# Performance work log

Measured on AMD Instinct MI355X. Metric: run time of the kernel, lower is better.

Reference implementation:

```python
import jax, jax.numpy as jnp
import numpy as np

N_NODES = 50000
N_EDGES = 800000
FEAT = 96


def _linear_params(key, din, dout):
    kw, kb = jax.random.split(key)
    scale = 1.0 / np.sqrt(din)
    W = jax.random.uniform(kw, (din, dout), jnp.float32, -scale, scale)
    b = jax.random.uniform(kb, (dout,), jnp.float32, -scale, scale)
    return W, b


def setup_inputs() -> dict:
    key = jax.random.key(0)
    ks = jax.random.split(key, 10)
    x = jax.random.normal(ks[0], (N_NODES, FEAT), jnp.float32)
    pos = jax.random.normal(ks[1], (N_NODES, 3), jnp.float32)
    edge_index = jax.random.randint(ks[2], (2, N_EDGES), 0, N_NODES, jnp.int64)
    # mlp_h: 96 -> 64 -> 3 (delta shift)
    h_w0, h_b0 = _linear_params(ks[3], FEAT, 64)
    h_w1, h_b1 = _linear_params(ks[4], 64, 3)
    # mlp_f: (96+3) -> 128 -> 96 (edge MLP)
    f_w0, f_b0 = _linear_params(ks[5], FEAT + 3, 128)
    f_w1, f_b1 = _linear_params(ks[6], 128, FEAT)
    # mlp_g: 96 -> 128 -> 96 (node update)
    g_w0, g_b0 = _linear_params(ks[7], FEAT, 128)
    g_w1, g_b1 = _linear_params(ks[8], 128, FEAT)
    return dict(x=x, pos=pos, edge_index=edge_index,
                h_w0=h_w0, h_b0=h_b0, h_w1=h_w1, h_b1=h_b1,
                f_w0=f_w0, f_b0=f_b0, f_w1=f_w1, f_b1=f_b1,
                g_w0=g_w0, g_b0=g_b0, g_w1=g_w1, g_b1=g_b1)


def _mlp2(h, w0, b0, w1, b1):
    # Linear -> ReLU -> Linear (output_activation='none')
    return jax.nn.relu(h @ w0 + b0) @ w1 + b1


def reference(x, pos, edge_index,
              h_w0, h_b0, h_w1, h_b1,
              f_w0, f_b0, f_w1, f_b1,
              g_w0, g_b0, g_w1, g_b1):
    src = edge_index[0]  # j: source / neighbor
    dst = edge_index[1]  # i: target
    # delta = mlp_h(x_i): learned shift of the center position
    delta = _mlp2(x, h_w0, h_b0, h_w1, h_b1)  # [N, 3]
    # per-edge feature: cat([pos_j - pos_i + delta_i, x_j])
    rel = pos[src] - pos[dst] + delta[dst]          # [E, 3]
    e_in = jnp.concatenate([rel, x[src]], axis=1)   # [E, 3+F]
    e = _mlp2(e_in, f_w0, f_b0, f_w1, f_b1)         # [E, F]
    # max-aggregate edges to target nodes (PointGNNConv aggr='max')
    agg = jax.ops.segment_max(e, dst, num_segments=N_NODES)
    agg = jnp.where(jnp.isneginf(agg), jnp.zeros_like(agg), agg)
    # residual node update
    return x + _mlp2(agg, g_w0, g_b0, g_w1, g_b1)
```

## Files before the change

kernel.cpp:

```cpp
#include <hip/hip_runtime.h>
#include <hip/hip_bf16.h>

typedef unsigned short u16;
typedef unsigned int u32;
typedef __bf16 bf16x8 __attribute__((ext_vector_type(8)));
typedef float f32x4 __attribute__((ext_vector_type(4)));

__device__ __forceinline__ float bf2f(u16 h) { return __uint_as_float(((u32)h) << 16); }
__device__ __forceinline__ u16 f2bf(float f) {
    u32 u = __float_as_uint(f);
    u32 r = u + 0x7FFFu + ((u >> 16) & 1u);
    return (u16)(r >> 16);
}
__device__ __forceinline__ u32 cvtpk(float lo, float hi) {
    u32 r;
    asm("v_cvt_pk_bf16_f32 %0, %1, %2" : "=v"(r) : "v"(lo), "v"(hi));
    return r;
}
__device__ __forceinline__ u16 cvt1(float v) { return (u16)cvtpk(v, v); }
__device__ __forceinline__ void unpack8(const u16* p, float* b) {
    uint4 v = *(const uint4*)p;
    b[0] = bf2f((u16)(v.x & 0xFFFF)); b[1] = bf2f((u16)(v.x >> 16));
    b[2] = bf2f((u16)(v.y & 0xFFFF)); b[3] = bf2f((u16)(v.y >> 16));
    b[4] = bf2f((u16)(v.z & 0xFFFF)); b[5] = bf2f((u16)(v.z >> 16));
    b[6] = bf2f((u16)(v.w & 0xFFFF)); b[7] = bf2f((u16)(v.w >> 16));
}
__device__ __forceinline__ float ldf(int bf, const void* p, long i) {
    return bf ? bf2f(((const u16*)p)[i]) : ((const float*)p)[i];
}

__global__ void k_detect(const u32* __restrict__ x, const u32* __restrict__ ei, u32* __restrict__ flags) {
    int tid = threadIdx.x;
    int c = 0;
    for (int i = tid; i < 256; i += 64) {
        u32 e = (x[i] >> 7) & 0xFF;
        if (e >= 96 && e <= 160) c++;
    }
#pragma unroll
    for (int d = 1; d < 64; d <<= 1) c += __shfl_xor(c, d);
    int z = (ei[2 * tid + 1] == 0u) ? 1 : 0;
#pragma unroll
    for (int d = 1; d < 64; d <<= 1) z += __shfl_xor(z, d);
    if (tid == 0) {
        flags[0] = (c >= 192) ? 1u : 0u;
        flags[1] = (z >= 48) ? 1u : 0u;
    }
}

__global__ void k_prep(const void* __restrict__ fw0, const void* __restrict__ fw1,
                       const void* __restrict__ gw0, const void* __restrict__ gw1,
                       const void* __restrict__ hw0,
                       u16* __restrict__ w0t, u16* __restrict__ w1t,
                       u16* __restrict__ w0tg, u16* __restrict__ w1tg, u16* __restrict__ hw0t,
                       const u32* __restrict__ flags,
                       u32* __restrict__ z1, int nz1, u32* __restrict__ z2, int nz2) {
    int bf = (int)flags[0];
    int tid = blockIdx.x * blockDim.x + threadIdx.x;
    int stride = gridDim.x * blockDim.x;
    for (int i = tid; i < nz1; i += stride) z1[i] = 0u;
    for (int i = tid; i < nz2; i += stride) z2[i] = 0u;
    for (int i = tid; i < 128 * 128; i += stride) {
        int c = i >> 7, kp = i & 127;
        float vf = (kp < 96) ? ldf(bf, fw0, (long)(kp + 3) * 128 + c) : 0.f;
        w0t[i] = f2bf(vf);
        float vg = (kp < 96) ? ldf(bf, gw0, (long)kp * 128 + c) : 0.f;
        w0tg[i] = f2bf(vg);
    }
    for (int i = tid; i < 96 * 128; i += stride) {
        int c = i >> 7, k = i & 127;
        w1t[i]  = f2bf(ldf(bf, fw1, (long)k * 96 + c));
        w1tg[i] = f2bf(ldf(bf, gw1, (long)k * 96 + c));
    }
    for (int i = tid; i < 64 * 128; i += stride) {
        int c = i >> 7, kp = i & 127;
        float v = (kp < 96) ? ldf(bf, hw0, (long)kp * 64 + c) : 0.f;
        hw0t[i] = f2bf(v);
    }
}

__global__ void k_cvt(const u32* __restrict__ ei, u32* __restrict__ eraw, u32* __restrict__ hist,
                      const u32* __restrict__ flags, int nE, int N) {
    u32 i64f = flags[1];
    for (long e = blockIdx.x * blockDim.x + threadIdx.x; e < nE; e += (long)gridDim.x * blockDim.x) {
        int src, dst;
        if (i64f) { src = (int)ei[2 * e]; dst = (int)ei[2 * ((long)nE + e)]; }
        else      { src = (int)ei[e];     dst = (int)ei[(long)nE + e]; }
        src = min(max(src, 0), N - 1);
        dst = min(max(dst, 0), N - 1);
        eraw[e] = (u32)src | ((u32)dst << 16);
        atomicAdd(&hist[dst], 1u);
    }
}

__global__ __launch_bounds__(256)
void k_scanA(const u32* __restrict__ hist, u32* __restrict__ blkSum, int n) {
    __shared__ u32 red[4];
    int tid = threadIdx.x;
    int base = blockIdx.x * 1024 + tid * 4;
    u32 s = 0;
#pragma unroll
    for (int j = 0; j < 4; j++) {
        int idx = base + j;
        if (idx < n) s += hist[idx];
    }
#pragma unroll
    for (int d = 1; d < 64; d <<= 1) s += __shfl_xor(s, d);
    if ((tid & 63) == 0) red[tid >> 6] = s;
    __syncthreads();
    if (tid == 0) blkSum[blockIdx.x] = red[0] + red[1] + red[2] + red[3];
}
__global__ __launch_bounds__(256)
void k_scanC(const u32* __restrict__ hist, const u32* __restrict__ blkSum,
             u32* __restrict__ cur, u32* __restrict__ dstart, int n, u32 total) {
    __shared__ u32 a[256];
    int tid = threadIdx.x;
    a[tid] = (tid < blockIdx.x) ? blkSum[tid] : 0u;
    __syncthreads();
    for (int d = 128; d > 0; d >>= 1) {
        if (tid < d) a[tid] += a[tid + d];
        __syncthreads();
    }
    u32 boff = a[0];
    __syncthreads();
    int base = blockIdx.x * 1024 + tid * 4;
    u32 e[4];
    u32 ts = 0;
#pragma unroll
    for (int j = 0; j < 4; j++) {
        int idx = base + j;
        e[j] = (idx < n) ? hist[idx] : 0u;
        ts += e[j];
    }
    a[tid] = ts;
    __syncthreads();
    for (int d = 1; d < 256; d <<= 1) {
        u32 t = (tid >= d) ? a[tid - d] : 0u;
        __syncthreads();
        a[tid] += t;
        __syncthreads();
    }
    u32 off = boff + a[tid] - ts;
#pragma unroll
    for (int j = 0; j < 4; j++) {
        int idx = base + j;
        if (idx < n) { cur[idx] = off; dstart[idx] = off; off += e[j]; }
    }
    if (blockIdx.x == 0 && tid == 0) dstart[n] = total;
}

__global__ void k_scatter(const u32* __restrict__ eraw, u32* __restrict__ cur,
                          u32* __restrict__ edges, int nE) {
    for (long e = blockIdx.x * blockDim.x + threadIdx.x; e < nE; e += (long)gridDim.x * blockDim.x) {
        u32 ed = eraw[e];
        u32 p = atomicAdd(&cur[ed >> 16], 1u);
        edges[p] = ed;
    }
}

__global__ __launch_bounds__(256)
void k_yd(const void* __restrict__ x, const void* __restrict__ pos,
          const u16* __restrict__ w0t, const u16* __restrict__ hw0t,
          const void* __restrict__ hb0, const void* __restrict__ hw1, const void* __restrict__ hb1,
          const void* __restrict__ fw0, const void* __restrict__ fb0,
          u16* __restrict__ yu, float* __restrict__ vbO,
          const u32* __restrict__ flags, int N)
{
    const int bf = (int)flags[0];
    __shared__ __align__(16) char arena[16384];
    __shared__ float posS[64][4];
    __shared__ float h1S[64][68];
    __shared__ float w0rS[384];
    __shared__ float b0fS[128];
    __shared__ float hb0S[64];
    __shared__ float hw1S[192];
    __shared__ float hb1S[3];
    int tid = threadIdx.x;
    for (int i = tid; i < 384; i += 256) w0rS[i] = ldf(bf, fw0, i);
    if (tid < 128) b0fS[tid] = ldf(bf, fb0, tid);
    if (tid < 64)  hb0S[tid] = ldf(bf, hb0, tid);
    if (tid < 192) hw1S[tid] = ldf(bf, hw1, tid);
    if (tid < 3)   hb1S[tid] = ldf(bf, hb1, tid);
    __syncthreads();

    const int lane = tid & 63;
    const int wid  = tid >> 6;
    const int mrow0 = wid * 16;
    const int r16  = lane & 15;
    const int arow = mrow0 + r16;
    const int kgrp = lane >> 4;
    const int srow = tid >> 2;
    const int q = tid & 3;
    const int ssw = (srow & 7) << 4;

    int ntile = (N + 63) / 64;
    for (int t = blockIdx.x; t < ntile; t += gridDim.x) {
        {
            int n = t * 64 + srow;
            if (tid < 64) {
                int n2 = t * 64 + tid;
                posS[tid][0] = (n2 < N) ? ldf(bf, pos, (long)n2 * 3 + 0) : 0.f;
                posS[tid][1] = (n2 < N) ? ldf(bf, pos, (long)n2 * 3 + 1) : 0.f;
                posS[tid][2] = (n2 < N) ? ldf(bf, pos, (long)n2 * 3 + 2) : 0.f;
            }
            if (n < N) {
                if (bf) {
                    const uint4* ar = (const uint4*)((const u16*)x + (size_t)n * 96);
#pragma unroll
                    for (int j = 0; j < 3; j++) {
                        int c = q * 3 + j;
                        *(uint4*)(arena + srow * 256 + ((c * 16) ^ ssw)) = ar[c];
                    }
                } else {
                    const float4* xp = (const float4*)((const float*)x + (size_t)n * 96);
#pragma unroll
                    for (int j = 0; j < 3; j++) {
                        int c = q * 3 + j;
                        float4 v0 = xp[2 * c], v1 = xp[2 * c + 1];
                        *(uint4*)(arena + srow * 256 + ((c * 16) ^ ssw)) =
                            make_uint4(cvtpk(v0.x, v0.y), cvtpk(v0.z, v0.w),
                                       cvtpk(v1.x, v1.y), cvtpk(v1.z, v1.w));
                    }
                }
            } else {
#pragma unroll
                for (int j = 0; j < 3; j++)
                    *(uint4*)(arena + srow * 256 + (((q * 3 + j) * 16) ^ ssw)) = make_uint4(0u, 0u, 0u, 0u);
            }
        }
        __syncthreads();
        int sw = (arow & 7) << 4;
        bf16x8 a0 = *(const bf16x8*)(arena + arow * 256 + ((0   + kgrp * 16) ^ sw));
        bf16x8 a1 = *(const bf16x8*)(arena + arow * 256 + ((64  + kgrp * 16) ^ sw));
        bf16x8 a2 = *(const bf16x8*)(arena + arow * 256 + ((128 + kgrp * 16) ^ sw));
        f32x4 accd[4];
#pragma unroll
        for (int nt = 0; nt < 4; nt++) {
#pragma unroll
            for (int r = 0; r < 4; r++) accd[nt][r] = 0.f;
        }
#pragma unroll
        for (int nt = 0; nt < 4; nt++) {
            const u16* wp = hw0t + (long)(nt * 16 + r16) * 128 + kgrp * 8;
            accd[nt] = __builtin_amdgcn_mfma_f32_16x16x32_bf16(a0, *(const bf16x8*)(wp),      accd[nt], 0, 0, 0);
            accd[nt] = __builtin_amdgcn_mfma_f32_16x16x32_bf16(a1, *(const bf16x8*)(wp + 32), accd[nt], 0, 0, 0);
            accd[nt] = __builtin_amdgcn_mfma_f32_16x16x32_bf16(a2, *(const bf16x8*)(wp + 64), accd[nt], 0, 0, 0);
        }
#pragma unroll
        for (int nt = 0; nt < 4; nt++) {
            int col = nt * 16 + r16;
#pragma unroll
            for (int r = 0; r < 4; r++)
                h1S[mrow0 + kgrp * 4 + r][col] = fmaxf(accd[nt][r] + hb0S[col], 0.f);
        }
        f32x4 acc[8];
#pragma unroll
        for (int nt = 0; nt < 8; nt++) {
#pragma unroll
            for (int r = 0; r < 4; r++) acc[nt][r] = 0.f;
        }
#pragma unroll
        for (int nt = 0; nt < 8; nt++) {
            const u16* wp = w0t + (long)(nt * 16 + r16) * 128 + kgrp * 8;
            acc[nt] = __builtin_amdgcn_mfma_f32_16x16x32_bf16(a0, *(const bf16x8*)(wp),      acc[nt], 0, 0, 0);
            acc[nt] = __builtin_amdgcn_mfma_f32_16x16x32_bf16(a1, *(const bf16x8*)(wp + 32), acc[nt], 0, 0, 0);
            acc[nt] = __builtin_amdgcn_mfma_f32_16x16x32_bf16(a2, *(const bf16x8*)(wp + 64), acc[nt], 0, 0, 0);
        }
        __syncthreads();
        {
            int nl = tid >> 2;
            int n = t * 64 + nl;
            float d0 = hb1S[0], d1 = hb1S[1], d2 = hb1S[2];
#pragma unroll 8
            for (int j = 0; j < 64; j++) {
                float hv = h1S[nl][j];
                d0 += hv * hw1S[j * 3 + 0];
                d1 += hv * hw1S[j * 3 + 1];
                d2 += hv * hw1S[j * 3 + 2];
            }
            float p0 = d0 - posS[nl][0], p1 = d1 - posS[nl][1], p2 = d2 - posS[nl][2];
            if (n < N) {
                float* vrow = vbO + (size_t)n * 128 + q * 32;
#pragma unroll
                for (int c4 = 0; c4 < 8; c4++) {
                    float4 o;
#pragma unroll
                    for (int k = 0; k < 4; k++) {
                        int col = q * 32 + c4 * 4 + k;
                        float v = p0 * w0rS[col] + p1 * w0rS[128 + col] + p2 * w0rS[256 + col] + b0fS[col];
                        ((float*)&o)[k] = v;
                    }
                    *(float4*)(vrow + c4 * 4) = o;
                }
            }
        }
#pragma unroll
        for (int nt = 0; nt < 8; nt++) {
            int col = nt * 16 + r16;
            float wr0 = w0rS[col], wr1 = w0rS[128 + col], wr2 = w0rS[256 + col];
#pragma unroll
            for (int r = 0; r < 4; r++) {
                int row = mrow0 + kgrp * 4 + r;
                int n2 = t * 64 + row;
                if (n2 < N) {
                    float u = posS[row][0] * wr0 + posS[row][1] * wr1 + posS[row][2] * wr2;
                    yu[(size_t)n2 * 128 + col] = cvt1(acc[nt][r] + u);
                }
            }
        }
        __syncthreads();
    }
}

__global__ __launch_bounds__(256)
void k_edge(const u16* __restrict__ yu, const float4* __restrict__ vb,
            const u32* __restrict__ edges, const u16* __restrict__ w1t,
            const void* __restrict__ fb1, const u32* __restrict__ flags,
            u16* __restrict__ agg, u16* __restrict__ pbuf, int nE)
{
    const int bf = (int)flags[0];
    __shared__ __align__(16) u16 w1S[96 * 128];
    __shared__ float b1s[96];
    __shared__ int dstS[4][16];
    __shared__ __align__(16) u16 outS[4][16 * 98];
    int tid = threadIdx.x;
    for (int i = tid; i < 96 * 64; i += 256) {
        int col = i >> 6, kp = i & 63;
        u32 v = ((const u32*)w1t)[i];
        *(u32*)((char*)w1S + col * 256 + ((kp * 4) ^ ((col & 7) << 4))) = v;
    }
    if (tid < 96) b1s[tid] = ldf(bf, fb1, tid);
    __syncthreads();

    const int lane = tid & 63;
    const int wid  = tid >> 6;
    const int r16  = lane & 15;
    const int kgrp = lane >> 4;
    const int ntile = (nE + 15) / 16;
    const size_t tailSlot = (size_t)ntile * 96;
    u16* const outSw = outS[wid];

    const int stride = (int)gridDim.x * 4;
    int t = (int)blockIdx.x * 4 + wid;

    u32 ce = 0u, ne = 0u;
    uint4 G[4];

    auto issueGather = [&](u32 src) {
        const u16* yp = yu + (size_t)src * 128 + kgrp * 8;
#pragma unroll
        for (int f = 0; f < 4; f++) G[f] = *(const uint4*)(yp + f * 32);
    };

    if (t < ntile) {
        long E = min((long)t * 16 + r16, (long)nE - 1);
        ce = edges[E];
        issueGather(ce & 0xFFFFu);
        int tn = t + stride;
        if (tn < ntile) {
            long En = min((long)tn * 16 + r16, (long)nE - 1);
            ne = edges[En];
        }
    }

    for (; t < ntile; t += stride) {
        asm volatile("" ::: "memory");
        if (kgrp == 3) dstS[wid][r16] = (int)(ce >> 16);
        int dprevV = -1, dnextV = -1;
        {
            long e0 = (long)t * 16;
            if (e0 > 0) dprevV = (int)(edges[e0 - 1] >> 16);
            if (e0 + 16 < (long)nE) dnextV = (int)(edges[e0 + 16] >> 16);
        }
        const float4* vbp = vb + (size_t)(ce >> 16) * 32 + kgrp * 2;
        bf16x8 hf[4];
#pragma unroll
        for (int f = 0; f < 4; f++) {
            float4 v0 = vbp[f * 8], v1 = vbp[f * 8 + 1];
            u32 w0 = G[f].x, w1 = G[f].y, w2 = G[f].z, w3 = G[f].w;
            u32 hw[4];
            hw[0] = cvtpk(fmaxf(bf2f((u16)(w0 & 0xFFFF)) + v0.x, 0.f),
                          fmaxf(bf2f((u16)(w0 >> 16))    + v0.y, 0.f));
            hw[1] = cvtpk(fmaxf(bf2f((u16)(w1 & 0xFFFF)) + v0.z, 0.f),
                          fmaxf(bf2f((u16)(w1 >> 16))    + v0.w, 0.f));
            hw[2] = cvtpk(fmaxf(bf2f((u16)(w2 & 0xFFFF)) + v1.x, 0.f),
                          fmaxf(bf2f((u16)(w2 >> 16))    + v1.y, 0.f));
            hw[3] = cvtpk(fmaxf(bf2f((u16)(w3 & 0xFFFF)) + v1.z, 0.f),
                          fmaxf(bf2f((u16)(w3 >> 16))    + v1.w, 0.f));
            uint4 hv = make_uint4(hw[0], hw[1], hw[2], hw[3]);
            hf[f] = *(const bf16x8*)&hv;
        }
        u32 c2e = ne;
        {
            int tn = t + stride;
            if (tn < ntile) {
                issueGather(c2e & 0xFFFFu);
                int tn2 = tn + stride;
                if (tn2 < ntile) {
                    long E2 = min((long)tn2 * 16 + r16, (long)nE - 1);
                    ne = edges[E2];
                }
            }
        }
        f32x4 acc2[6];
#pragma unroll
        for (int nt = 0; nt < 6; nt++) {
#pragma unroll
            for (int r = 0; r < 4; r++) acc2[nt][r] = 0.f;
        }
#pragma unroll
        for (int nt = 0; nt < 6; nt++) {
            int colr = nt * 16 + r16;
            const char* wb = (const char*)w1S + colr * 256;
            int csw = (colr & 7) << 4;
            acc2[nt] = __builtin_amdgcn_mfma_f32_16x16x32_bf16(hf[0], *(const bf16x8*)(wb + ((kgrp * 16)       ^ csw)), acc2[nt], 0, 0, 0);
            acc2[nt] = __builtin_amdgcn_mfma_f32_16x16x32_bf16(hf[1], *(const bf16x8*)(wb + ((kgrp * 16 + 64)  ^ csw)), acc2[nt], 0, 0, 0);
            acc2[nt] = __builtin_amdgcn_mfma_f32_16x16x32_bf16(hf[2], *(const bf16x8*)(wb + ((kgrp * 16 + 128) ^ csw)), acc2[nt], 0, 0, 0);
            acc2[nt] = __builtin_amdgcn_mfma_f32_16x16x32_bf16(hf[3], *(const bf16x8*)(wb + ((kgrp * 16 + 192) ^ csw)), acc2[nt], 0, 0, 0);
        }
#pragma unroll
        for (int nt = 0; nt < 6; nt++) {
            int col = nt * 16 + r16;
#pragma unroll
            for (int r = 0; r < 4; r++) {
                int row = kgrp * 4 + r;
                outSw[row * 98 + col] = cvt1(acc2[nt][r]);
            }
        }
        {
            int d0s = dstS[wid][0], d15s = dstS[wid][15];
            bool extL = (dprevV == d0s);
            bool extR = (dnextV == d15s);
#pragma unroll
            for (int p = 0; p < 2; p++) {
                int col = p * 64 + lane;
                if (p == 0 || lane < 32) {
                    float b1c = b1s[col];
                    int curd = d0s;
                    int r0 = 0;
                    float m = bf2f(outSw[col]);
#pragma unroll
                    for (int row = 1; row < 16; row++) {
                        float v = bf2f(outSw[row * 98 + col]);
                        int d = dstS[wid][row];
                        if (d != curd) {
                            if (r0 == 0 && extL) pbuf[(size_t)t * 96 + col] = cvt1(m);
                            else agg[(size_t)curd * 96 + col] = cvt1(m + b1c);
                            curd = d; r0 = row; m = v;
                        } else m = fmaxf(m, v);
                    }
                    bool pl = (r0 == 0) && extL;
                    if (pl || extR) {
                        size_t slot = (r0 == 0) ? 0 : tailSlot;
                        pbuf[slot + (size_t)t * 96 + col] = cvt1(m);
                    } else agg[(size_t)curd * 96 + col] = cvt1(m + b1c);
                }
            }
        }
        ce = c2e;
    }
}

__global__ __launch_bounds__(256)
void k_node(const void* __restrict__ x, const u16* __restrict__ agg,
            const u32* __restrict__ dstart, const u16* __restrict__ pbuf,
            const u16* __restrict__ w0tg, const u16* __restrict__ w1tg,
            const void* __restrict__ gb0, const void* __restrict__ gb1,
            const void* __restrict__ fb1,
            void* __restrict__ out, const u32* __restrict__ flags, int N, int nE)
{
    const int bf = (int)flags[0];
    __shared__ __align__(16) char arena[32768];
    __shared__ float b0s[128];
    __shared__ float b1s[96];
    __shared__ float b1f[96];
    int tid = threadIdx.x;
    if (tid < 128) b0s[tid] = ldf(bf, gb0, tid);
    if (tid < 96)  b1s[tid] = ldf(bf, gb1, tid);
    if (tid < 96)  b1f[tid] = ldf(bf, fb1, tid);
    __syncthreads();

    const int lane = tid & 63;
    const int wid  = tid >> 6;
    const int mrow0 = wid * 16;
    const int arow = mrow0 + (lane & 15);
    const int kgrp = lane >> 4;
    const int srow = tid >> 2;
    const int q = tid & 3;
    const int ssw = (srow & 7) << 4;
    const int ntileE = (nE + 15) / 16;

    float b0v[8];
#pragma unroll
    for (int nt = 0; nt < 8; nt++) b0v[nt] = b0s[nt * 16 + (lane & 15)];

    auto outOff = [](int row, int col) {
        int j = row & 15, w2 = row >> 4;
        int base = (j < 8) ? (w2 * 4096 + j * 512) : (16384 + w2 * 4096 + (j - 8) * 512);
        return base + ((col ^ (((row >> 2) & 3) << 4)) << 2);
    };

    int ntile = (N + 63) / 64;
    for (int t = blockIdx.x; t < ntile; t += gridDim.x) {
        asm volatile("" ::: "memory");
        {
            int n = t * 64 + srow;
            if (n < N) {
                u32 s = dstart[n], e = dstart[n + 1];
                int t0 = (int)(s >> 4);
                int t1 = (e > s) ? (int)((e - 1) >> 4) : t0;
                if (e > s && t0 != t1) {
                    const u16* pH = pbuf;
                    const u16* pT = pbuf + (size_t)ntileE * 96;
                    const u16* first = ((s & 15u) == 0u) ? pH : pT;
#pragma unroll
                    for (int j = 0; j < 3; j++) {
                        int c = q * 3 + j;
                        float mf[8];
                        unpack8(first + (size_t)t0 * 96 + c * 8, mf);
                        for (int tt = t0 + 1; tt <= t1; tt++) {
                            float tf[8];
                            unpack8(pH + (size_t)tt * 96 + c * 8, tf);
#pragma unroll
                            for (int k = 0; k < 8; k++) mf[k] = fmaxf(mf[k], tf[k]);
                        }
                        uint4 o;
                        o.x = cvtpk(mf[0] + b1f[c * 8 + 0], mf[1] + b1f[c * 8 + 1]);
                        o.y = cvtpk(mf[2] + b1f[c * 8 + 2], mf[3] + b1f[c * 8 + 3]);
                        o.z = cvtpk(mf[4] + b1f[c * 8 + 4], mf[5] + b1f[c * 8 + 5]);
                        o.w = cvtpk(mf[6] + b1f[c * 8 + 6], mf[7] + b1f[c * 8 + 7]);
                        *(uint4*)(arena + srow * 256 + ((c * 16) ^ ssw)) = o;
                    }
                } else {
                    const uint4* ar = (const uint4*)(agg + (size_t)n * 96);
#pragma unroll
                    for (int j = 0; j < 3; j++) {
                        int c = q * 3 + j;
                        *(uint4*)(arena + srow * 256 + ((c * 16) ^ ssw)) = ar[c];
                    }
                }
            } else {
#pragma unroll
                for (int j = 0; j < 3; j++)
                    *(uint4*)(arena + srow * 256 + (((q * 3 + j) * 16) ^ ssw)) = make_uint4(0u, 0u, 0u, 0u);
            }
        }
        __syncthreads();
        int sw = (arow & 7) << 4;
        bf16x8 a0 = *(const bf16x8*)(arena + arow * 256 + ((0   + kgrp * 16) ^ sw));
        bf16x8 a1 = *(const bf16x8*)(arena + arow * 256 + ((64  + kgrp * 16) ^ sw));
        bf16x8 a2 = *(const bf16x8*)(arena + arow * 256 + ((128 + kgrp * 16) ^ sw));
        f32x4 acc[8];
#pragma unroll
        for (int nt = 0; nt < 8; nt++) {
#pragma unroll
            for (int r = 0; r < 4; r++) acc[nt][r] = 0.f;
        }
#pragma unroll
        for (int nt = 0; nt < 8; nt++) {
            const u16* wp = w0tg + (long)(nt * 16 + (lane & 15)) * 128 + kgrp * 8;
            acc[nt] = __builtin_amdgcn_mfma_f32_16x16x32_bf16(a0, *(const bf16x8*)(wp),      acc[nt], 0, 0, 0);
            acc[nt] = __builtin_amdgcn_mfma_f32_16x16x32_bf16(a1, *(const bf16x8*)(wp + 32), acc[nt], 0, 0, 0);
            acc[nt] = __builtin_amdgcn_mfma_f32_16x16x32_bf16(a2, *(const bf16x8*)(wp + 64), acc[nt], 0, 0, 0);
        }
#pragma unroll
        for (int nt = 0; nt < 8; nt++) {
            int col = nt * 16 + (lane & 15);
#pragma unroll
            for (int r = 0; r < 4; r++) {
                int row = mrow0 + kgrp * 4 + r;
                float hv = fmaxf(acc[nt][r] + b0v[nt], 0.f);
                *(u16*)(arena + 16384 + row * 256 + ((col * 2) ^ ((row & 7) << 4))) = cvt1(hv);
            }
        }
        bf16x8 h0 = *(const bf16x8*)(arena + 16384 + arow * 256 + ((0   + kgrp * 16) ^ sw));
        bf16x8 h1 = *(const bf16x8*)(arena + 16384 + arow * 256 + ((64  + kgrp * 16) ^ sw));
        bf16x8 h2 = *(const bf16x8*)(arena + 16384 + arow * 256 + ((128 + kgrp * 16) ^ sw));
        bf16x8 h3 = *(const bf16x8*)(arena + 16384 + arow * 256 + ((192 + kgrp * 16) ^ sw));
        f32x4 acc2[6];
#pragma unroll
        for (int nt = 0; nt < 6; nt++) {
#pragma unroll
            for (int r = 0; r < 4; r++) acc2[nt][r] = 0.f;
        }
#pragma unroll
        for (int nt = 0; nt < 6; nt++) {
            const u16* wp = w1tg + (long)(nt * 16 + (lane & 15)) * 128 + kgrp * 8;
            acc2[nt] = __builtin_amdgcn_mfma_f32_16x16x32_bf16(h0, *(const bf16x8*)(wp),      acc2[nt], 0, 0, 0);
            acc2[nt] = __builtin_amdgcn_mfma_f32_16x16x32_bf16(h1, *(const bf16x8*)(wp + 32), acc2[nt], 0, 0, 0);
            acc2[nt] = __builtin_amdgcn_mfma_f32_16x16x32_bf16(h2, *(const bf16x8*)(wp + 64), acc2[nt], 0, 0, 0);
            acc2[nt] = __builtin_amdgcn_mfma_f32_16x16x32_bf16(h3, *(const bf16x8*)(wp + 96), acc2[nt], 0, 0, 0);
        }
#pragma unroll
        for (int nt = 0; nt < 6; nt++) {
            int col = nt * 16 + (lane & 15);
#pragma unroll
            for (int r = 0; r < 4; r++) {
                int row = mrow0 + kgrp * 4 + r;
                *(float*)(arena + outOff(row, col)) = acc2[nt][r];
            }
        }
        __syncthreads();
        {
            int n = t * 64 + srow;
            if (n < N) {
                float v[24];
#pragma unroll
                for (int c = 0; c < 24; c++) v[c] = *(const float*)(arena + outOff(srow, q * 24 + c));
                if (bf) {
                    u16* orow = (u16*)out + (size_t)n * 96 + q * 24;
#pragma unroll
                    for (int j = 0; j < 3; j++) {
                        float xv[8];
                        unpack8((const u16*)x + (size_t)n * 96 + q * 24 + j * 8, xv);
                        uint4 o;
                        o.x = cvtpk(xv[0] + v[j * 8 + 0] + b1s[q * 24 + j * 8 + 0],
                                    xv[1] + v[j * 8 + 1] + b1s[q * 24 + j * 8 + 1]);
                        o.y = cvtpk(xv[2] + v[j * 8 + 2] + b1s[q * 24 + j * 8 + 2],
                                    xv[3] + v[j * 8 + 3] + b1s[q * 24 + j * 8 + 3]);
                        o.z = cvtpk(xv[4] + v[j * 8 + 4] + b1s[q * 24 + j * 8 + 4],
                                    xv[5] + v[j * 8 + 5] + b1s[q * 24 + j * 8 + 5]);
                        o.w = cvtpk(xv[6] + v[j * 8 + 6] + b1s[q * 24 + j * 8 + 6],
                                    xv[7] + v[j * 8 + 7] + b1s[q * 24 + j * 8 + 7]);
                        *(uint4*)(orow + j * 8) = o;
                    }
                } else {
                    const float* xr = (const float*)x + (size_t)n * 96 + q * 24;
                    float* orow = (float*)out + (size_t)n * 96 + q * 24;
#pragma unroll
                    for (int j = 0; j < 6; j++) {
                        float4 xv = ((const float4*)xr)[j];
                        float4 o;
                        o.x = xv.x + v[4 * j + 0] + b1s[q * 24 + 4 * j + 0];
                        o.y = xv.y + v[4 * j + 1] + b1s[q * 24 + 4 * j + 1];
                        o.z = xv.z + v[4 * j + 2] + b1s[q * 24 + 4 * j + 2];
                        o.w = xv.w + v[4 * j + 3] + b1s[q * 24 + 4 * j + 3];
                        ((float4*)orow)[j] = o;
                    }
                }
            }
        }
        __syncthreads();
    }
}

extern "C" void kernel_launch(void* const* d_in, const int* in_sizes, int n_in,
                              void* d_out, int out_size, void* d_ws, size_t ws_size,
                              hipStream_t stream) {
    const void* x   = d_in[0];
    const void* pos = d_in[1];
    const void* ei  = d_in[2];
    const void* hw0 = d_in[3];
    const void* hb0 = d_in[4];
    const void* hw1 = d_in[5];
    const void* hb1 = d_in[6];
    const void* fw0 = d_in[7];
    const void* fb0 = d_in[8];
    const void* fw1 = d_in[9];
    const void* fb1 = d_in[10];
    const void* gw0 = d_in[11];
    const void* gb0 = d_in[12];
    const void* gw1 = d_in[13];
    const void* gb1 = d_in[14];

    int N  = in_sizes[0] / 96;
    int nE = in_sizes[2] / 2;
    int ntileE = (nE + 15) / 16;
    int nBlkScan = (N + 1023) / 1024;

    size_t off = 0;
    auto alloc = [&](size_t bytes) { size_t o = off; off = (off + bytes + 255) & ~(size_t)255; return o; };
    u32*    flags    = (u32*)((char*)d_ws + alloc(256));
    u16*    w0t      = (u16*)((char*)d_ws + alloc(128 * 128 * 2));
    u16*    w1t      = (u16*)((char*)d_ws + alloc(96 * 128 * 2));
    u16*    w0tg     = (u16*)((char*)d_ws + alloc(128 * 128 * 2));
    u16*    w1tg     = (u16*)((char*)d_ws + alloc(96 * 128 * 2));
    u16*    hw0t     = (u16*)((char*)d_ws + alloc(64 * 128 * 2));
    u32*    binCur   = (u32*)((char*)d_ws + alloc((size_t)N * 4));
    u32*    dstStart = (u32*)((char*)d_ws + alloc((size_t)(N + 1) * 4));
    u32*    blkSum   = (u32*)((char*)d_ws + alloc((size_t)(nBlkScan + 1) * 4));
    u16*    agg      = (u16*)((char*)d_ws + alloc((size_t)N * 96 * 2));
    u32*    eraw     = (u32*)((char*)d_ws + alloc((size_t)nE * 4));
    u32*    edges    = (u32*)((char*)d_ws + alloc((size_t)nE * 4));
    u16*    pbuf     = (u16*)((char*)d_ws + alloc((size_t)2 * ntileE * 96 * 2));
    u16*    yubuf    = (u16*)((char*)d_ws + alloc((size_t)N * 128 * 2));
    float*  vbbuf    = (float*)((char*)d_ws + alloc((size_t)N * 128 * 4));

    k_detect<<<1, 64, 0, stream>>>((const u32*)x, (const u32*)ei, flags);
    k_prep<<<256, 256, 0, stream>>>(fw0, fw1, gw0, gw1, hw0, w0t, w1t, w0tg, w1tg, hw0t,
                                    flags, (u32*)agg, N * 48, binCur, N);
    k_cvt<<<1024, 256, 0, stream>>>((const u32*)ei, eraw, binCur, flags, nE, N);
    k_scanA<<<nBlkScan, 256, 0, stream>>>(binCur, blkSum, N);
    k_scanC<<<nBlkScan, 256, 0, stream>>>(binCur, blkSum, binCur, dstStart, N, (u32)nE);
    k_scatter<<<1024, 256, 0, stream>>>(eraw, binCur, edges, nE);
    int yGrid = (N + 63) / 64;
    k_yd<<<yGrid, 256, 0, stream>>>(x, pos, w0t, hw0t, hb0, hw1, hb1, fw0, fb0,
                                    yubuf, vbbuf, flags, N);
    k_edge<<<1024, 256, 0, stream>>>(yubuf, (const float4*)vbbuf, edges, w1t, fb1, flags,
                                     agg, pbuf, nE);
    k_node<<<yGrid, 256, 0, stream>>>(x, agg, dstStart, pbuf, w0tg, w1tg, gb0, gb1, fb1,
                                      d_out, flags, N, nE);
}
```

Baseline: 359.6 us.

## Fuse detect into prep, single-pass scan, rank-based scatter fused into node MLP

Folds format detection into the weight-prep kernel, which every block now recomputes locally. It replaces the two-pass scan with one kernel where each block re-sums all preceding histogram entries, and records each edge's atomic rank during counting. That rank lets the scatter run without atomics inside the node-MLP kernel. Together this cuts three kernel launches and one atomic pass. In exchange it adds a rank buffer, redundant prefix summation, and extra scatter work at the start of the per-node kernel.

```diff
diff --git a/kernel.cpp b/kernel.cpp
--- a/kernel.cpp
+++ b/kernel.cpp
@@ -29,57 +29,57 @@
     return bf ? bf2f(((const u16*)p)[i]) : ((const float*)p)[i];
 }
 
-__global__ void k_detect(const u32* __restrict__ x, const u32* __restrict__ ei, u32* __restrict__ flags) {
-    int tid = threadIdx.x;
-    int c = 0;
-    for (int i = tid; i < 256; i += 64) {
-        u32 e = (x[i] >> 7) & 0xFF;
-        if (e >= 96 && e <= 160) c++;
-    }
-#pragma unroll
-    for (int d = 1; d < 64; d <<= 1) c += __shfl_xor(c, d);
-    int z = (ei[2 * tid + 1] == 0u) ? 1 : 0;
-#pragma unroll
-    for (int d = 1; d < 64; d <<= 1) z += __shfl_xor(z, d);
-    if (tid == 0) {
-        flags[0] = (c >= 192) ? 1u : 0u;
-        flags[1] = (z >= 48) ? 1u : 0u;
-    }
-}
-
-__global__ void k_prep(const void* __restrict__ fw0, const void* __restrict__ fw1,
+__global__ void k_prep(const u32* __restrict__ xw, const u32* __restrict__ eiw,
+                       const void* __restrict__ fw0, const void* __restrict__ fw1,
                        const void* __restrict__ gw0, const void* __restrict__ gw1,
                        const void* __restrict__ hw0,
                        u16* __restrict__ w0t, u16* __restrict__ w1t,
                        u16* __restrict__ w0tg, u16* __restrict__ w1tg, u16* __restrict__ hw0t,
-                       const u32* __restrict__ flags,
+                       u32* __restrict__ flags,
                        u32* __restrict__ z1, int nz1, u32* __restrict__ z2, int nz2) {
-    int bf = (int)flags[0];
-    int tid = blockIdx.x * blockDim.x + threadIdx.x;
+    __shared__ u32 fl[2];
+    int tid = threadIdx.x;
+    if (tid < 64) {
+        int c = 0;
+        for (int i = tid; i < 256; i += 64) {
+            u32 e = (xw[i] >> 7) & 0xFF;
+            if (e >= 96 && e <= 160) c++;
+        }
+#pragma unroll
+        for (int d = 1; d < 64; d <<= 1) c += __shfl_xor(c, d);
+        int z = (eiw[2 * tid + 1] == 0u) ? 1 : 0;
+#pragma unroll
+        for (int d = 1; d < 64; d <<= 1) z += __shfl_xor(z, d);
+        if (tid == 0) { fl[0] = (c >= 192) ? 1u : 0u; fl[1] = (z >= 48) ? 1u : 0u; }
+    }
+    __syncthreads();
+    const int bf = (int)fl[0];
+    if (blockIdx.x == 0 && tid == 0) { flags[0] = fl[0]; flags[1] = fl[1]; }
+    int gid = blockIdx.x * blockDim.x + tid;
     int stride = gridDim.x * blockDim.x;
-    for (int i = tid; i < nz1; i += stride) z1[i] = 0u;
-    for (int i = tid; i < nz2; i += stride) z2[i] = 0u;
-    for (int i = tid; i < 128 * 128; i += stride) {
+    for (int i = gid; i < nz1; i += stride) z1[i] = 0u;
+    for (int i = gid; i < nz2; i += stride) z2[i] = 0u;
+    for (int i = gid; i < 128 * 128; i += stride) {
         int c = i >> 7, kp = i & 127;
         float vf = (kp < 96) ? ldf(bf, fw0, (long)(kp + 3) * 128 + c) : 0.f;
         w0t[i] = f2bf(vf);
         float vg = (kp < 96) ? ldf(bf, gw0, (long)kp * 128 + c) : 0.f;
         w0tg[i] = f2bf(vg);
     }
-    for (int i = tid; i < 96 * 128; i += stride) {
+    for (int i = gid; i < 96 * 128; i += stride) {
         int c = i >> 7, k = i & 127;
         w1t[i]  = f2bf(ldf(bf, fw1, (long)k * 96 + c));
         w1tg[i] = f2bf(ldf(bf, gw1, (long)k * 96 + c));
     }
-    for (int i = tid; i < 64 * 128; i += stride) {
+    for (int i = gid; i < 64 * 128; i += stride) {
         int c = i >> 7, kp = i & 127;
         float v = (kp < 96) ? ldf(bf, hw0, (long)kp * 64 + c) : 0.f;
         hw0t[i] = f2bf(v);
     }
 }
 
-__global__ void k_cvt(const u32* __restrict__ ei, u32* __restrict__ eraw, u32* __restrict__ hist,
-                      const u32* __restrict__ flags, int nE, int N) {
+__global__ void k_cvt(const u32* __restrict__ ei, u32* __restrict__ eraw, u32* __restrict__ rank,
+                      u32* __restrict__ hist, const u32* __restrict__ flags, int nE, int N) {
     u32 i64f = flags[1];
     for (long e = blockIdx.x * blockDim.x + threadIdx.x; e < nE; e += (long)gridDim.x * blockDim.x) {
         int src, dst;
@@ -88,33 +88,18 @@
         src = min(max(src, 0), N - 1);
         dst = min(max(dst, 0), N - 1);
         eraw[e] = (u32)src | ((u32)dst << 16);
-        atomicAdd(&hist[dst], 1u);
+        rank[e] = atomicAdd(&hist[dst], 1u);
     }
 }
 
 __global__ __launch_bounds__(256)
-void k_scanA(const u32* __restrict__ hist, u32* __restrict__ blkSum, int n) {
-    __shared__ u32 red[4];
-    int tid = threadIdx.x;
-    int base = blockIdx.x * 1024 + tid * 4;
-    u32 s = 0;
-#pragma unroll
-    for (int j = 0; j < 4; j++) {
-        int idx = base + j;
-        if (idx < n) s += hist[idx];
-    }
-#pragma unroll
-    for (int d = 1; d < 64; d <<= 1) s += __shfl_xor(s, d);
-    if ((tid & 63) == 0) red[tid >> 6] = s;
-    __syncthreads();
-    if (tid == 0) blkSum[blockIdx.x] = red[0] + red[1] + red[2] + red[3];
-}
-__global__ __launch_bounds__(256)
-void k_scanC(const u32* __restrict__ hist, const u32* __restrict__ blkSum,
-             u32* __restrict__ cur, u32* __restrict__ dstart, int n, u32 total) {
+void k_scanF(const u32* __restrict__ hist, u32* __restrict__ dstart, int n, u32 total) {
     __shared__ u32 a[256];
     int tid = threadIdx.x;
-    a[tid] = (tid < blockIdx.x) ? blkSum[tid] : 0u;
+    long lim = (long)blockIdx.x << 10;
+    u32 s0 = 0;
+    for (long i = tid; i < lim; i += 256) s0 += hist[i];
+    a[tid] = s0;
     __syncthreads();
     for (int d = 128; d > 0; d >>= 1) {
         if (tid < d) a[tid] += a[tid + d];
@@ -122,14 +107,14 @@
     }
     u32 boff = a[0];
     __syncthreads();
-    int base = blockIdx.x * 1024 + tid * 4;
-    u32 e[4];
+    int base = (int)(blockIdx.x << 10) + tid * 4;
+    u32 e4[4];
     u32 ts = 0;
 #pragma unroll
     for (int j = 0; j < 4; j++) {
         int idx = base + j;
-        e[j] = (idx < n) ? hist[idx] : 0u;
-        ts += e[j];
+        e4[j] = (idx < n) ? hist[idx] : 0u;
+        ts += e4[j];
     }
     a[tid] = ts;
     __syncthreads();
@@ -143,27 +128,20 @@
 #pragma unroll
     for (int j = 0; j < 4; j++) {
         int idx = base + j;
-        if (idx < n) { cur[idx] = off; dstart[idx] = off; off += e[j]; }
+        if (idx < n) { dstart[idx] = off; off += e4[j]; }
     }
     if (blockIdx.x == 0 && tid == 0) dstart[n] = total;
 }
 
-__global__ void k_scatter(const u32* __restrict__ eraw, u32* __restrict__ cur,
-                          u32* __restrict__ edges, int nE) {
-    for (long e = blockIdx.x * blockDim.x + threadIdx.x; e < nE; e += (long)gridDim.x * blockDim.x) {
-        u32 ed = eraw[e];
-        u32 p = atomicAdd(&cur[ed >> 16], 1u);
-        edges[p] = ed;
-    }
-}
-
 __global__ __launch_bounds__(256)
-void k_yd(const void* __restrict__ x, const void* __restrict__ pos,
-          const u16* __restrict__ w0t, const u16* __restrict__ hw0t,
-          const void* __restrict__ hb0, const void* __restrict__ hw1, const void* __restrict__ hb1,
-          const void* __restrict__ fw0, const void* __restrict__ fb0,
-          u16* __restrict__ yu, float* __restrict__ vbO,
-          const u32* __restrict__ flags, int N)
+void k_ydsc(const void* __restrict__ x, const void* __restrict__ pos,
+            const u16* __restrict__ w0t, const u16* __restrict__ hw0t,
+            const void* __restrict__ hb0, const void* __restrict__ hw1, const void* __restrict__ hb1,
+            const void* __restrict__ fw0, const void* __restrict__ fb0,
+            u16* __restrict__ yu, float* __restrict__ vbO,
+            const u32* __restrict__ flags, int N,
+            const u32* __restrict__ eraw, const u32* __restrict__ rank,
+            const u32* __restrict__ dstart, u32* __restrict__ edges, int nE)
 {
     const int bf = (int)flags[0];
     __shared__ __align__(16) char arena[16384];
@@ -175,6 +153,13 @@
     __shared__ float hw1S[192];
     __shared__ float hb1S[3];
     int tid = threadIdx.x;
+    {
+        long stride = (long)gridDim.x * 256;
+        for (long e = (long)blockIdx.x * 256 + tid; e < nE; e += stride) {
+            u32 ed = eraw[e];
+            edges[dstart[ed >> 16] + rank[e]] = ed;
+        }
+    }
     for (int i = tid; i < 384; i += 256) w0rS[i] = ldf(bf, fw0, i);
     if (tid < 128) b0fS[tid] = ldf(bf, fb0, tid);
     if (tid < 64)  hb0S[tid] = ldf(bf, hb0, tid);
@@ -675,28 +660,26 @@
     u16*    w0tg     = (u16*)((char*)d_ws + alloc(128 * 128 * 2));
     u16*    w1tg     = (u16*)((char*)d_ws + alloc(96 * 128 * 2));
     u16*    hw0t     = (u16*)((char*)d_ws + alloc(64 * 128 * 2));
-    u32*    binCur   = (u32*)((char*)d_ws + alloc((size_t)N * 4));
-    u32*    dstStart = (u32*)((char*)d_ws + alloc((size_t)(N + 1) * 4));
-    u32*    blkSum   = (u32*)((char*)d_ws + alloc((size_t)(nBlkScan + 1) * 4));
+    u32*    hist     = (u32*)((char*)d_ws + alloc((size_t)N * 4));
+    u32*    dstart   = (u32*)((char*)d_ws + alloc((size_t)(N + 1) * 4));
     u16*    agg      = (u16*)((char*)d_ws + alloc((size_t)N * 96 * 2));
     u32*    eraw     = (u32*)((char*)d_ws + alloc((size_t)nE * 4));
+    u32*    rank     = (u32*)((char*)d_ws + alloc((size_t)nE * 4));
     u32*    edges    = (u32*)((char*)d_ws + alloc((size_t)nE * 4));
     u16*    pbuf     = (u16*)((char*)d_ws + alloc((size_t)2 * ntileE * 96 * 2));
     u16*    yubuf    = (u16*)((char*)d_ws + alloc((size_t)N * 128 * 2));
     float*  vbbuf    = (float*)((char*)d_ws + alloc((size_t)N * 128 * 4));
 
-    k_detect<<<1, 64, 0, stream>>>((const u32*)x, (const u32*)ei, flags);
-    k_prep<<<256, 256, 0, stream>>>(fw0, fw1, gw0, gw1, hw0, w0t, w1t, w0tg, w1tg, hw0t,
-                                    flags, (u32*)agg, N * 48, binCur, N);
-    k_cvt<<<1024, 256, 0, stream>>>((const u32*)ei, eraw, binCur, flags, nE, N);
-    k_scanA<<<nBlkScan, 256, 0, stream>>>(binCur, blkSum, N);
-    k_scanC<<<nBlkScan, 256, 0, stream>>>(binCur, blkSum, binCur, dstStart, N, (u32)nE);
-    k_scatter<<<1024, 256, 0, stream>>>(eraw, binCur, edges, nE);
+    k_prep<<<1024, 256, 0, stream>>>((const u32*)x, (const u32*)ei, fw0, fw1, gw0, gw1, hw0,
+                                     w0t, w1t, w0tg, w1tg, hw0t, flags,
+                                     (u32*)agg, N * 48, hist, N);
+    k_cvt<<<1024, 256, 0, stream>>>((const u32*)ei, eraw, rank, hist, flags, nE, N);
+    k_scanF<<<nBlkScan, 256, 0, stream>>>(hist, dstart, N, (u32)nE);
     int yGrid = (N + 63) / 64;
-    k_yd<<<yGrid, 256, 0, stream>>>(x, pos, w0t, hw0t, hb0, hw1, hb1, fw0, fb0,
-                                    yubuf, vbbuf, flags, N);
+    k_ydsc<<<yGrid, 256, 0, stream>>>(x, pos, w0t, hw0t, hb0, hw1, hb1, fw0, fb0,
+                                      yubuf, vbbuf, flags, N, eraw, rank, dstart, edges, nE);
     k_edge<<<1024, 256, 0, stream>>>(yubuf, (const float4*)vbbuf, edges, w1t, fb1, flags,
                                      agg, pbuf, nE);
-    k_node<<<yGrid, 256, 0, stream>>>(x, agg, dstStart, pbuf, w0tg, w1tg, gb0, gb1, fb1,
+    k_node<<<yGrid, 256, 0, stream>>>(x, agg, dstart, pbuf, w0tg, w1tg, gb0, gb1, fb1,
                                       d_out, flags, N, nE);
 }
```

Result: faster. 331.1 us (median of 2 runs) (-7.9%).
